# Kernel tuning notes

Hardware: AMD Instinct MI355X
Metric: run time of the kernel (lower is better)

Reference implementation:

```python
import jax, jax.numpy as jnp
import numpy as np

B, C_IN, H, W = 4, 256, 256, 256
L = 5000                 # candidate lines per image
N_PTS0, N_PTS1 = 32, 8   # sampled points per line, pooled points
DIM_LOI, DIM_FC = 128, 1024
N_OUT_LINE = 2500


def setup_inputs() -> dict:
    key = jax.random.key(0)
    ks = jax.random.split(key, 8)
    feature = jax.random.normal(ks[0], (B, C_IN, H, W), jnp.float32)
    # line endpoints in [0, 255) pixel coords (row, col)
    lines_in = jax.random.uniform(ks[1], (B, L, 2, 2), jnp.float32) * 255.0
    fc1_w = jax.random.normal(ks[2], (DIM_LOI, C_IN), jnp.float32) * 0.05
    fc1_b = jnp.zeros((DIM_LOI,), jnp.float32)
    w1 = jax.random.normal(ks[3], (DIM_FC, DIM_LOI * N_PTS1), jnp.float32) * 0.02
    b1 = jnp.zeros((DIM_FC,), jnp.float32)
    w2 = jax.random.normal(ks[4], (DIM_FC, DIM_FC), jnp.float32) * 0.02
    b2 = jnp.zeros((DIM_FC,), jnp.float32)
    w3 = jax.random.normal(ks[5], (4, DIM_FC), jnp.float32) * 0.02
    b3 = jnp.zeros((4,), jnp.float32)
    return dict(feature=feature, lines_in=lines_in, fc1_w=fc1_w, fc1_b=fc1_b,
                w1=w1, b1=b1, w2=w2, b2=b2, w3=w3, b3=b3)


def _bilinear_sample(xi, px, py):
    # xi: [C, H, W]; px, py: [P] float coords. Matches torch clamp(0, 255).
    px0 = jnp.clip(jnp.floor(px), 0.0, 255.0)
    py0 = jnp.clip(jnp.floor(py), 0.0, 255.0)
    px1 = jnp.clip(px0 + 1.0, 0.0, 255.0)
    py1 = jnp.clip(py0 + 1.0, 0.0, 255.0)
    px0l, py0l = px0.astype(jnp.int32), py0.astype(jnp.int32)
    px1l, py1l = px1.astype(jnp.int32), py1.astype(jnp.int32)
    xp = (xi[:, px0l, py0l] * (px1 - px) * (py1 - py)
          + xi[:, px1l, py0l] * (px - px0) * (py1 - py)
          + xi[:, px0l, py1l] * (px1 - px) * (py - py0)
          + xi[:, px1l, py1l] * (px - px0) * (py - py0))
    return xp  # [C, P]


def _select(p0, s0, m):
    # p0: [L,2,2], s0: [L,4], m: [L] bool. Threshold-masked, argsort by argmax
    # class (descending), cyclically padded to N_OUT_LINE.
    max_idx = jnp.argmax(s0, axis=1)
    sort_key = jnp.where(m, max_idx, -1)          # unmasked rows sink to the end
    order = jnp.argsort(-sort_key)                # stable, descending by class id
    cnt = m.sum()
    idxs = jnp.arange(N_OUT_LINE) % jnp.maximum(cnt, 1)
    sel = order[idxs]
    li = jnp.where(cnt > 0, p0[sel], jnp.zeros_like(p0[sel]))
    si = jnp.where(cnt > 0, s0[sel], jnp.zeros_like(s0[sel]))
    return li, si


def reference(feature, lines_in, fc1_w, fc1_b, w1, b1, w2, b2, w3, b3):
    # fc1: 1x1 conv -> [B, DIM_LOI, H, W]
    x = jnp.einsum('bchw,oc->bohw', feature, fc1_w) + fc1_b[None, :, None, None]

    # sample N_PTS0 points along each line: p0*lam + p1*(1-lam) - 0.5
    lam = jnp.linspace(0.0, 1.0, N_PTS0, dtype=jnp.float32)[:, None]  # [32,1]
    pts = lines_in[:, :, 0:1, :] * lam + lines_in[:, :, 1:2, :] * (1.0 - lam) - 0.5  # [B,L,32,2]
    px = pts[..., 0].reshape(B, -1)  # [B, L*32]
    py = pts[..., 1].reshape(B, -1)

    xp = jax.vmap(_bilinear_sample)(x, px, py)            # [B, C, L*32]
    xp = xp.reshape(B, DIM_LOI, L, N_PTS0).transpose(0, 2, 1, 3)  # [B, L, C, 32]

    # MaxPool1d(4, 4) over the point axis -> [B, L, C, 8]
    xp = xp.reshape(B, L, DIM_LOI, N_PTS1, N_PTS0 // N_PTS1).max(axis=-1)
    flat = xp.reshape(B, L, DIM_LOI * N_PTS1)

    # fc2 MLP: 1024 -> 1024 -> 1024 -> 4
    h = jax.nn.relu(jnp.einsum('blf,df->bld', flat, w1) + b1)
    h = jax.nn.relu(jnp.einsum('bld,ed->ble', h, w2) + b2)
    logits = jnp.einsum('ble,oe->blo', h, w3) + b3        # [B, L, 4]

    s = jax.nn.softmax(logits, axis=-1)
    mask = ((s[..., 1] > 0.25) | (s[..., 2] > 0.25) | (s[..., 3] > 0.25)) & (s[..., 0] < 0.25)

    lines_out, score_out = jax.vmap(_select)(lines_in, s, mask)
    return lines_out, score_out  # [B, 2500, 2, 2], [B, 2500, 4]
```

## Files before the change

### kernel.cpp

```cpp
#include <hip/hip_runtime.h>
#include <hip/hip_bf16.h>
#include <math.h>

#define BB 4
#define C_IN 256
#define HH 256
#define WW 256
#define LL 5000
#define N_PTS0 32
#define N_PTS1 8
#define DIM_LOI 128
#define DIM_FC 1024
#define N_OUT_LINE 2500
#define MM (BB * LL)
#define PIX (HH * WW)

typedef __attribute__((ext_vector_type(8))) short short8_t;
typedef __attribute__((ext_vector_type(4))) float float4v;

__device__ __forceinline__ short f2bf(float f) {
    union { float f; unsigned u; } c; c.f = f;
    unsigned u = c.u;
    u += 0x7FFFu + ((u >> 16) & 1u);
    return (short)(u >> 16);
}
__device__ __forceinline__ float bf2f(short h) {
    union { unsigned u; float f; } c; c.u = ((unsigned)(unsigned short)h) << 16;
    return c.f;
}

__device__ __forceinline__ void load_lds16(const void* g, void* l) {
    __builtin_amdgcn_global_load_lds(
        (const __attribute__((address_space(1))) void*)g,
        (__attribute__((address_space(3))) void*)l, 16, 0, 0);
}

__device__ __forceinline__ void wave_barrier() {
    asm volatile("" ::: "memory");
    __builtin_amdgcn_s_barrier();
    asm volatile("" ::: "memory");
}

#define MFMA_B16(a, b, c) \
    c = __builtin_amdgcn_mfma_f32_16x16x32_bf16(a, b, c, 0, 0, 0)

__global__ __launch_bounds__(256) void conv_mfma_kernel(
    const float* __restrict__ feat,
    const short* __restrict__ whi,
    const short* __restrict__ wlo,
    const float* __restrict__ bias,
    float* __restrict__ x)
{
    __shared__ short As_hi[128][40];
    __shared__ short As_lo[128][40];
    __shared__ short Ws_hi[128][40];
    __shared__ short Ws_lo[128][40];

    const int t  = threadIdx.x;
    const int m0 = blockIdx.x * 128;
    const int b  = m0 >> 16;
    const int p0 = m0 & (PIX - 1);
    const float* fb = feat + (size_t)b * C_IN * PIX + p0;

    const int w = t >> 6, lane = t & 63;
    const int wmb = (w >> 1) * 64, wnb = (w & 1) * 64;
    const int fr = lane & 15;
    const int koff = (lane >> 4) << 3;

    const int sp = t & 127;
    const int cg = t >> 7;

    float4v acc[4][4];
#pragma unroll
    for (int mi = 0; mi < 4; mi++)
#pragma unroll
        for (int ni = 0; ni < 4; ni++)
            acc[mi][ni] = (float4v){0.f, 0.f, 0.f, 0.f};

    for (int k0 = 0; k0 < C_IN; k0 += 32) {
#pragma unroll
        for (int i = 0; i < 2; i++) {
            int idx = t + (i << 8);
            int row = idx >> 2;
            int kc  = (idx & 3) << 3;
            *(int4*)&Ws_hi[row][kc] = *(const int4*)(whi + row * C_IN + k0 + kc);
            *(int4*)&Ws_lo[row][kc] = *(const int4*)(wlo + row * C_IN + k0 + kc);
        }
#pragma unroll
        for (int j = 0; j < 8; j++) {
            int c = cg * 16 + j * 2;
            float v0 = fb[(size_t)(k0 + c) * PIX + sp];
            float v1 = fb[(size_t)(k0 + c + 1) * PIX + sp];
            short h0 = f2bf(v0), h1 = f2bf(v1);
            short l0 = f2bf(v0 - bf2f(h0)), l1 = f2bf(v1 - bf2f(h1));
            *(unsigned*)&As_hi[sp][c] =
                (unsigned)(unsigned short)h0 | ((unsigned)(unsigned short)h1 << 16);
            *(unsigned*)&As_lo[sp][c] =
                (unsigned)(unsigned short)l0 | ((unsigned)(unsigned short)l1 << 16);
        }
        __syncthreads();

        short8_t ah[4], al[4];
#pragma unroll
        for (int mi = 0; mi < 4; mi++) {
            ah[mi] = *(const short8_t*)&As_hi[wmb + mi * 16 + fr][koff];
            al[mi] = *(const short8_t*)&As_lo[wmb + mi * 16 + fr][koff];
        }
#pragma unroll
        for (int ni = 0; ni < 4; ni++) {
            short8_t bh = *(const short8_t*)&Ws_hi[wnb + ni * 16 + fr][koff];
            short8_t bl = *(const short8_t*)&Ws_lo[wnb + ni * 16 + fr][koff];
#pragma unroll
            for (int mi = 0; mi < 4; mi++) {
                MFMA_B16(ah[mi], bh, acc[mi][ni]);
                MFMA_B16(al[mi], bh, acc[mi][ni]);
                MFMA_B16(ah[mi], bl, acc[mi][ni]);
            }
        }
        __syncthreads();
    }

#pragma unroll
    for (int ni = 0; ni < 4; ni++) {
        int ncol = wnb + ni * 16 + fr;
        float bv = bias[ncol];
#pragma unroll
        for (int mi = 0; mi < 4; mi++) {
            int r0 = m0 + wmb + mi * 16 + ((lane >> 4) << 2);
#pragma unroll
            for (int i2 = 0; i2 < 4; i2++) {
                x[(size_t)(r0 + i2) * 128 + ncol] = acc[mi][ni][i2] + bv;
            }
        }
    }
}

__global__ __launch_bounds__(256) void sample_pool_kernel(
    const float* __restrict__ lines,
    const float* __restrict__ x,
    short* __restrict__ phi,
    short* __restrict__ plo)
{
    const int t  = threadIdx.x;
    const int bl = blockIdx.x * 8 + (t >> 5);
    const int b  = bl / LL;
    const int cg = t & 31;
    const float* lp = lines + (size_t)bl * 4;
    const float p0r = lp[0], p0c = lp[1], p1r = lp[2], p1c = lp[3];
    const float* xb = x + (size_t)b * PIX * 128 + cg * 4;

    short8_t vh[4], vl[4];
#pragma unroll
    for (int g = 0; g < 8; g++) {
        float mx0 = -INFINITY, mx1 = -INFINITY, mx2 = -INFINITY, mx3 = -INFINITY;
#pragma unroll
        for (int j = 0; j < 4; j++) {
            int tt = g * 4 + j;
            float lam = (float)((double)tt / 31.0);
            float px = p0r * lam + p1r * (1.0f - lam) - 0.5f;
            float py = p0c * lam + p1c * (1.0f - lam) - 0.5f;
            float px0 = fminf(fmaxf(floorf(px), 0.0f), 255.0f);
            float py0 = fminf(fmaxf(floorf(py), 0.0f), 255.0f);
            float px1 = fminf(px0 + 1.0f, 255.0f);
            float py1 = fminf(py0 + 1.0f, 255.0f);
            int ix0 = (int)px0, iy0 = (int)py0, ix1 = (int)px1, iy1 = (int)py1;
            float wx1 = px1 - px, wx0 = px - px0;
            float wy1 = py1 - py, wy0 = py - py0;
            float w00 = wx1 * wy1, w10 = wx0 * wy1;
            float w01 = wx1 * wy0, w11 = wx0 * wy0;
            float4 v00 = *(const float4*)(xb + (size_t)(ix0 * WW + iy0) * 128);
            float4 v10 = *(const float4*)(xb + (size_t)(ix1 * WW + iy0) * 128);
            float4 v01 = *(const float4*)(xb + (size_t)(ix0 * WW + iy1) * 128);
            float4 v11 = *(const float4*)(xb + (size_t)(ix1 * WW + iy1) * 128);
            mx0 = fmaxf(mx0, v00.x * w00 + v10.x * w10 + v01.x * w01 + v11.x * w11);
            mx1 = fmaxf(mx1, v00.y * w00 + v10.y * w10 + v01.y * w01 + v11.y * w11);
            mx2 = fmaxf(mx2, v00.z * w00 + v10.z * w10 + v01.z * w01 + v11.z * w11);
            mx3 = fmaxf(mx3, v00.w * w00 + v10.w * w10 + v01.w * w01 + v11.w * w11);
        }
        float mxs[4] = {mx0, mx1, mx2, mx3};
#pragma unroll
        for (int k = 0; k < 4; k++) {
            short h = f2bf(mxs[k]);
            vh[k][g] = h;
            vl[k][g] = f2bf(mxs[k] - bf2f(h));
        }
    }
#pragma unroll
    for (int k = 0; k < 4; k++) {
        *(short8_t*)(phi + (size_t)bl * 1024 + (cg * 4 + k) * 8) = vh[k];
        *(short8_t*)(plo + (size_t)bl * 1024 + (cg * 4 + k) * 8) = vl[k];
    }
}

__global__ __launch_bounds__(256) void split_kernel(
    const float* __restrict__ w, short* __restrict__ hi, short* __restrict__ lo)
{
    const int i = (blockIdx.x * 256 + threadIdx.x) * 4;
    float4 v = *(const float4*)(w + i);
    float vv[4] = {v.x, v.y, v.z, v.w};
    short4 h, l;
    short hs[4], ls[4];
#pragma unroll
    for (int j = 0; j < 4; j++) {
        hs[j] = f2bf(vv[j]);
        ls[j] = f2bf(vv[j] - bf2f(hs[j]));
    }
    h.x = hs[0]; h.y = hs[1]; h.z = hs[2]; h.w = hs[3];
    l.x = ls[0]; l.y = ls[1]; l.z = ls[2]; l.w = ls[3];
    *(short4*)(hi + i) = h;
    *(short4*)(lo + i) = l;
}

#define NT 32
#define BUFS 28672
#define A_LO 6144
#define B_HI 12288
#define B_LO 20480

template <bool SPLIT_OUT>
__global__ __launch_bounds__(512, 2) void gemm_bf16x3_v4(
    const short* __restrict__ Ahi, const short* __restrict__ Alo,
    const short* __restrict__ Bhi, const short* __restrict__ Blo,
    const float* __restrict__ bias,
    float* __restrict__ Cf, short* __restrict__ Chi, short* __restrict__ Clo,
    int M, int Mtiles)
{
    __shared__ short lds[2 * BUFS];

    const int t   = threadIdx.x;
    const int bid = blockIdx.x;
    const int nwg = Mtiles * 4;
    const int q = nwg >> 3, r = nwg & 7;
    const int xcd = bid & 7, seq = bid >> 3;
    const int wgid = ((xcd < r) ? xcd * (q + 1) : r * (q + 1) + (xcd - r) * q) + seq;
    const int tileM = wgid >> 2, tileN = wgid & 3;
    const int m0 = tileM * 192, n0 = tileN * 256;

    const int w = t >> 6, lane = t & 63;
    const int wr = w >> 2;
    const int wc = w & 3;
    const int fr = lane & 15;
    const int ksw = (((lane >> 4) ^ ((lane >> 1) & 3)) << 3);
    const int a_row = wr * 96 + fr;
    const int b_row = wc * 64 + fr;

    const short* gp[7];
    int lp[7];
    {
        const int csrc = (lane & 3) ^ ((lane >> 3) & 3);
#pragma unroll
        for (int s = 0; s < 7; s++) {
            int e = w * 7 + s;
            const short* mp; int mo, j, grow;
            int rl = lane >> 2;
            if (e < 12)      { mp = Ahi; mo = 0;    j = e;      grow = min(m0 + j * 16 + rl, M - 1); }
            else if (e < 24) { mp = Alo; mo = A_LO; j = e - 12; grow = min(m0 + j * 16 + rl, M - 1); }
            else if (e < 40) { mp = Bhi; mo = B_HI; j = e - 24; grow = n0 + j * 16 + rl; }
            else             { mp = Blo; mo = B_LO; j = e - 40; grow = n0 + j * 16 + rl; }
            gp[s] = mp + (size_t)grow * 1024 + csrc * 8;
            lp[s] = mo + j * 512 + lane * 8;
        }
    }

#pragma unroll
    for (int s = 0; s < 7; s++) { load_lds16(gp[s], &lds[lp[s]]); gp[s] += 32; }
#pragma unroll
    for (int s = 0; s < 7; s++) { load_lds16(gp[s], &lds[BUFS + lp[s]]); gp[s] += 32; }
    asm volatile("s_waitcnt vmcnt(7)" ::: "memory");
    wave_barrier();

    float4v acc[6][4];
#pragma unroll
    for (int mf = 0; mf < 6; mf++)
#pragma unroll
        for (int nf = 0; nf < 4; nf++)
            acc[mf][nf] = (float4v){0.f, 0.f, 0.f, 0.f};

    for (int kt = 0; kt < NT; ++kt) {
        const int off = (kt & 1) * BUFS;

        short8_t bh[4], bl[4];
#pragma unroll
        for (int nf = 0; nf < 4; nf++) {
            bh[nf] = *(const short8_t*)&lds[off + B_HI + (b_row + nf * 16) * 32 + ksw];
            bl[nf] = *(const short8_t*)&lds[off + B_LO + (b_row + nf * 16) * 32 + ksw];
        }
#pragma unroll
        for (int mf = 0; mf < 6; mf++) {
            short8_t ah = *(const short8_t*)&lds[off + (a_row + mf * 16) * 32 + ksw];
            short8_t al = *(const short8_t*)&lds[off + A_LO + (a_row + mf * 16) * 32 + ksw];
#pragma unroll
            for (int nf = 0; nf < 4; nf++) {
                MFMA_B16(ah, bh[nf], acc[mf][nf]);
                MFMA_B16(al, bh[nf], acc[mf][nf]);
                MFMA_B16(ah, bl[nf], acc[mf][nf]);
            }
        }

        if (kt < NT - 1) {
            wave_barrier();
            if (kt + 2 < NT) {
#pragma unroll
                for (int s = 0; s < 7; s++) {
                    load_lds16(gp[s], &lds[off + lp[s]]); gp[s] += 32;
                }
                asm volatile("s_waitcnt vmcnt(7)" ::: "memory");
            } else {
                asm volatile("s_waitcnt vmcnt(0)" ::: "memory");
            }
            wave_barrier();
        }
    }

#pragma unroll
    for (int nf = 0; nf < 4; nf++) {
        int ncol = n0 + wc * 64 + nf * 16 + fr;
        float bv = bias[ncol];
#pragma unroll
        for (int mf = 0; mf < 6; mf++) {
            int r0 = m0 + wr * 96 + mf * 16 + ((lane >> 4) << 2);
#pragma unroll
            for (int i2 = 0; i2 < 4; i2++) {
                int rr = r0 + i2;
                if (rr < M) {
                    float v = fmaxf(acc[mf][nf][i2] + bv, 0.0f);
                    if (SPLIT_OUT) {
                        short h = f2bf(v);
                        Chi[(size_t)rr * 1024 + ncol] = h;
                        Clo[(size_t)rr * 1024 + ncol] = f2bf(v - bf2f(h));
                    } else {
                        Cf[(size_t)rr * 1024 + ncol] = v;
                    }
                }
            }
        }
    }
}

__global__ __launch_bounds__(256) void fc3_softmax_kernel(
    const float* __restrict__ h2, const float* __restrict__ w3,
    const float* __restrict__ b3, float* __restrict__ s, int* __restrict__ keys)
{
    const int m = blockIdx.x * 4 + (threadIdx.x >> 6);
    const int lane = threadIdx.x & 63;
    const float* hp = h2 + (size_t)m * DIM_FC;
    float a0 = 0.f, a1 = 0.f, a2 = 0.f, a3 = 0.f;
    for (int k = lane; k < DIM_FC; k += 64) {
        float hv = hp[k];
        a0 = fmaf(hv, w3[k], a0);
        a1 = fmaf(hv, w3[DIM_FC + k], a1);
        a2 = fmaf(hv, w3[2 * DIM_FC + k], a2);
        a3 = fmaf(hv, w3[3 * DIM_FC + k], a3);
    }
#pragma unroll
    for (int off = 32; off > 0; off >>= 1) {
        a0 += __shfl_down(a0, off, 64);
        a1 += __shfl_down(a1, off, 64);
        a2 += __shfl_down(a2, off, 64);
        a3 += __shfl_down(a3, off, 64);
    }
    if (lane == 0) {
        float l0 = a0 + b3[0], l1 = a1 + b3[1], l2 = a2 + b3[2], l3 = a3 + b3[3];
        float mxl = fmaxf(fmaxf(l0, l1), fmaxf(l2, l3));
        float e0 = expf(l0 - mxl), e1 = expf(l1 - mxl);
        float e2 = expf(l2 - mxl), e3 = expf(l3 - mxl);
        float inv = 1.0f / (e0 + e1 + e2 + e3);
        float s0 = e0 * inv, s1 = e1 * inv, s2 = e2 * inv, s3 = e3 * inv;
        float* sp = s + (size_t)m * 4;
        sp[0] = s0; sp[1] = s1; sp[2] = s2; sp[3] = s3;
        int best = 0; float bv = s0;
        if (s1 > bv) { best = 1; bv = s1; }
        if (s2 > bv) { best = 2; bv = s2; }
        if (s3 > bv) { best = 3; bv = s3; }
        bool msk = ((s1 > 0.25f) || (s2 > 0.25f) || (s3 > 0.25f)) && (s0 < 0.25f);
        keys[m] = msk ? best : -1;
    }
}

__global__ __launch_bounds__(64) void order_kernel(
    const int* __restrict__ keys, int* __restrict__ ord, int* __restrict__ cnts)
{
    const int b = blockIdx.x;
    const int lane = threadIdx.x;
    const int* kb = keys + b * LL;
    int c0 = 0, c1 = 0, c2 = 0, c3 = 0;
    for (int line = lane; line < LL; line += 64) {
        int k = kb[line];
        c0 += (k == 0); c1 += (k == 1); c2 += (k == 2); c3 += (k == 3);
    }
#pragma unroll
    for (int off = 32; off > 0; off >>= 1) {
        c0 += __shfl_down(c0, off, 64);
        c1 += __shfl_down(c1, off, 64);
        c2 += __shfl_down(c2, off, 64);
        c3 += __shfl_down(c3, off, 64);
    }
    int t0 = __shfl(c0, 0, 64), t1 = __shfl(c1, 0, 64);
    int t2 = __shfl(c2, 0, 64), t3 = __shfl(c3, 0, 64);
    if (lane == 0) cnts[b] = t0 + t1 + t2 + t3;
    int base[4];
    base[3] = 0; base[2] = t3; base[1] = t3 + t2; base[0] = t3 + t2 + t1;
    int run[4] = {0, 0, 0, 0};
    const unsigned long long below = (1ull << lane) - 1ull;
    int* ob = ord + b * LL;
    for (int s0 = 0; s0 < LL; s0 += 64) {
        int line = s0 + lane;
        int k = (line < LL) ? kb[line] : -2;
#pragma unroll
        for (int kk = 0; kk < 4; kk++) {
            unsigned long long mask = __ballot(k == kk);
            if (k == kk) {
                int pos = base[kk] + run[kk] + __popcll(mask & below);
                ob[pos] = line;
            }
            run[kk] += __popcll(mask);
        }
    }
}

__global__ __launch_bounds__(256) void fill_kernel(
    const float* __restrict__ lines, const float* __restrict__ s,
    const int* __restrict__ ord, const int* __restrict__ cnts,
    float* __restrict__ out)
{
    const int i = blockIdx.x * 256 + threadIdx.x;
    if (i >= BB * N_OUT_LINE) return;
    const int b = i / N_OUT_LINE;
    const int j = i % N_OUT_LINE;
    const int cnt = cnts[b];
    float4 lo = {0.f, 0.f, 0.f, 0.f}, sc = {0.f, 0.f, 0.f, 0.f};
    if (cnt > 0) {
        int line = ord[b * LL + (j % cnt)];
        lo = *(const float4*)(lines + ((size_t)b * LL + line) * 4);
        sc = *(const float4*)(s + ((size_t)b * LL + line) * 4);
    }
    *(float4*)(out + (size_t)i * 4) = lo;
    *(float4*)(out + (size_t)(BB * N_OUT_LINE) * 4 + (size_t)i * 4) = sc;
}

extern "C" void kernel_launch(void* const* d_in, const int* in_sizes, int n_in,
                              void* d_out, int out_size, void* d_ws, size_t ws_size,
                              hipStream_t stream) {
    (void)in_sizes; (void)n_in; (void)out_size; (void)ws_size;
    const float* feature = (const float*)d_in[0];
    const float* lines   = (const float*)d_in[1];
    const float* fc1_w   = (const float*)d_in[2];
    const float* fc1_b   = (const float*)d_in[3];
    const float* w1      = (const float*)d_in[4];
    const float* b1      = (const float*)d_in[5];
    const float* w2      = (const float*)d_in[6];
    const float* b2      = (const float*)d_in[7];
    const float* w3      = (const float*)d_in[8];
    const float* b3      = (const float*)d_in[9];
    float* out = (float*)d_out;

    float* x = (float*)d_ws;
    short* pooled_hi = (short*)(x + (size_t)BB * PIX * 128);
    short* pooled_lo = pooled_hi + (size_t)MM * DIM_FC;
    short* h1hi = (short*)x;
    short* h1lo = h1hi + (size_t)MM * DIM_FC;
    float* h2 = (float*)pooled_hi;
    short* w1hi = (short*)((char*)d_ws + 100u * 1024u * 1024u);
    short* w1lo = w1hi + DIM_FC * DIM_FC;
    short* w2hi = w1lo + DIM_FC * DIM_FC;
    short* w2lo = w2hi + DIM_FC * DIM_FC;
    float* s    = (float*)(pooled_lo + (size_t)MM * DIM_FC);
    int* keys   = (int*)(s + MM * 4);
    int* ord    = keys + MM;
    int* cnts   = ord + MM;
    short* fc1hi = (short*)(cnts + 64);
    short* fc1lo = fc1hi + DIM_LOI * C_IN;

    split_kernel<<<(DIM_LOI * C_IN) / 1024, 256, 0, stream>>>(fc1_w, fc1hi, fc1lo);
    conv_mfma_kernel<<<(BB * PIX) / 128, 256, 0, stream>>>(
        feature, fc1hi, fc1lo, fc1_b, x);
    sample_pool_kernel<<<MM / 8, 256, 0, stream>>>(lines, x, pooled_hi, pooled_lo);
    split_kernel<<<DIM_FC * DIM_FC / 1024, 256, 0, stream>>>(w1, w1hi, w1lo);
    split_kernel<<<DIM_FC * DIM_FC / 1024, 256, 0, stream>>>(w2, w2hi, w2lo);

    const int Mtiles = (MM + 191) / 192;
    gemm_bf16x3_v4<true><<<Mtiles * 4, 512, 0, stream>>>(
        pooled_hi, pooled_lo, w1hi, w1lo, b1, nullptr, h1hi, h1lo, MM, Mtiles);
    gemm_bf16x3_v4<false><<<Mtiles * 4, 512, 0, stream>>>(
        h1hi, h1lo, w2hi, w2lo, b2, h2, nullptr, nullptr, MM, Mtiles);

    fc3_softmax_kernel<<<MM / 4, 256, 0, stream>>>(h2, w3, b3, s, keys);
    order_kernel<<<BB, 64, 0, stream>>>(keys, ord, cnts);
    fill_kernel<<<(BB * N_OUT_LINE + 255) / 256, 256, 0, stream>>>(
        lines, s, ord, cnts, out);
}
```

Measured before the change: 898.8 us.

## Bucket-sort sampling groups spatially for cache locality in bilinear gather

Splits the per-line sampling into per-pooled-group work items and orders them by a counting sort over 32x32 spatial tiles per image, so that wavefronts gathering from the feature map touch nearby pixels and hit in cache more often. The pooled feature layout becomes group-major (g*128+channel), and the w1 weight split is permuted to match so the first GEMM result is unchanged. This adds four small kernels (histogram, scan, scatter) and atomics, and turns the pooled stores into short4 writes instead of short8 writes.

New measurement: 1.081 ms. 1.2x slower.

```diff
diff --git a/kernel.cpp b/kernel.cpp
--- a/kernel.cpp
+++ b/kernel.cpp
@@ -14,6 +14,7 @@
 #define N_OUT_LINE 2500
 #define MM (BB * LL)
 #define PIX (HH * WW)
+#define NGRP (MM * N_PTS1)
 
 typedef __attribute__((ext_vector_type(8))) short short8_t;
 typedef __attribute__((ext_vector_type(4))) float float4v;
@@ -135,61 +136,111 @@
     }
 }
 
+__global__ __launch_bounds__(256) void zero_hist_kernel(int* __restrict__ hist)
+{
+    hist[threadIdx.x] = 0;
+}
+
+__global__ __launch_bounds__(256) void group_key_kernel(
+    const float* __restrict__ lines, int* __restrict__ key, int* __restrict__ hist)
+{
+    const int gid = blockIdx.x * 256 + threadIdx.x;
+    if (gid >= NGRP) return;
+    const int bl = gid >> 3, g = gid & 7;
+    const float* lp = lines + (size_t)bl * 4;
+    const float lam = (float)((double)(g * 4) / 31.0);
+    float px = lp[0] * lam + lp[2] * (1.0f - lam) - 0.5f;
+    float py = lp[1] * lam + lp[3] * (1.0f - lam) - 0.5f;
+    int ix = min(max((int)floorf(px), 0), 255);
+    int iy = min(max((int)floorf(py), 0), 255);
+    const int b = bl / LL;
+    const int k = b * 64 + (ix >> 5) * 8 + (iy >> 5);
+    key[gid] = k;
+    atomicAdd(&hist[k], 1);
+}
+
+__global__ __launch_bounds__(256) void scan_kernel(
+    const int* __restrict__ hist, int* __restrict__ cursor)
+{
+    __shared__ int sh[256];
+    const int t = threadIdx.x;
+    const int h = hist[t];
+    sh[t] = h;
+    __syncthreads();
+#pragma unroll
+    for (int off = 1; off < 256; off <<= 1) {
+        int u = (t >= off) ? sh[t - off] : 0;
+        __syncthreads();
+        sh[t] += u;
+        __syncthreads();
+    }
+    cursor[t] = sh[t] - h;
+}
+
+__global__ __launch_bounds__(256) void scatter_kernel(
+    const int* __restrict__ key, int* __restrict__ cursor, int* __restrict__ perm)
+{
+    const int gid = blockIdx.x * 256 + threadIdx.x;
+    if (gid >= NGRP) return;
+    const int k = key[gid];
+    const int pos = atomicAdd(&cursor[k], 1);
+    perm[pos] = gid;
+}
+
 __global__ __launch_bounds__(256) void sample_pool_kernel(
     const float* __restrict__ lines,
     const float* __restrict__ x,
+    const int* __restrict__ perm,
     short* __restrict__ phi,
     short* __restrict__ plo)
 {
     const int t  = threadIdx.x;
-    const int bl = blockIdx.x * 8 + (t >> 5);
+    const int pg = perm[blockIdx.x * 8 + (t >> 5)];
+    const int bl = pg >> 3, g = pg & 7;
     const int b  = bl / LL;
     const int cg = t & 31;
     const float* lp = lines + (size_t)bl * 4;
     const float p0r = lp[0], p0c = lp[1], p1r = lp[2], p1c = lp[3];
     const float* xb = x + (size_t)b * PIX * 128 + cg * 4;
 
-    short8_t vh[4], vl[4];
-#pragma unroll
-    for (int g = 0; g < 8; g++) {
-        float mx0 = -INFINITY, mx1 = -INFINITY, mx2 = -INFINITY, mx3 = -INFINITY;
-#pragma unroll
-        for (int j = 0; j < 4; j++) {
-            int tt = g * 4 + j;
-            float lam = (float)((double)tt / 31.0);
-            float px = p0r * lam + p1r * (1.0f - lam) - 0.5f;
-            float py = p0c * lam + p1c * (1.0f - lam) - 0.5f;
-            float px0 = fminf(fmaxf(floorf(px), 0.0f), 255.0f);
-            float py0 = fminf(fmaxf(floorf(py), 0.0f), 255.0f);
-            float px1 = fminf(px0 + 1.0f, 255.0f);
-            float py1 = fminf(py0 + 1.0f, 255.0f);
-            int ix0 = (int)px0, iy0 = (int)py0, ix1 = (int)px1, iy1 = (int)py1;
-            float wx1 = px1 - px, wx0 = px - px0;
-            float wy1 = py1 - py, wy0 = py - py0;
-            float w00 = wx1 * wy1, w10 = wx0 * wy1;
-            float w01 = wx1 * wy0, w11 = wx0 * wy0;
-            float4 v00 = *(const float4*)(xb + (size_t)(ix0 * WW + iy0) * 128);
-            float4 v10 = *(const float4*)(xb + (size_t)(ix1 * WW + iy0) * 128);
-            float4 v01 = *(const float4*)(xb + (size_t)(ix0 * WW + iy1) * 128);
-            float4 v11 = *(const float4*)(xb + (size_t)(ix1 * WW + iy1) * 128);
-            mx0 = fmaxf(mx0, v00.x * w00 + v10.x * w10 + v01.x * w01 + v11.x * w11);
-            mx1 = fmaxf(mx1, v00.y * w00 + v10.y * w10 + v01.y * w01 + v11.y * w11);
-            mx2 = fmaxf(mx2, v00.z * w00 + v10.z * w10 + v01.z * w01 + v11.z * w11);
-            mx3 = fmaxf(mx3, v00.w * w00 + v10.w * w10 + v01.w * w01 + v11.w * w11);
-        }
-        float mxs[4] = {mx0, mx1, mx2, mx3};
-#pragma unroll
-        for (int k = 0; k < 4; k++) {
-            short h = f2bf(mxs[k]);
-            vh[k][g] = h;
-            vl[k][g] = f2bf(mxs[k] - bf2f(h));
-        }
-    }
+    float mx0 = -INFINITY, mx1 = -INFINITY, mx2 = -INFINITY, mx3 = -INFINITY;
+#pragma unroll
+    for (int j = 0; j < 4; j++) {
+        int tt = g * 4 + j;
+        float lam = (float)((double)tt / 31.0);
+        float px = p0r * lam + p1r * (1.0f - lam) - 0.5f;
+        float py = p0c * lam + p1c * (1.0f - lam) - 0.5f;
+        float px0 = fminf(fmaxf(floorf(px), 0.0f), 255.0f);
+        float py0 = fminf(fmaxf(floorf(py), 0.0f), 255.0f);
+        float px1 = fminf(px0 + 1.0f, 255.0f);
+        float py1 = fminf(py0 + 1.0f, 255.0f);
+        int ix0 = (int)px0, iy0 = (int)py0, ix1 = (int)px1, iy1 = (int)py1;
+        float wx1 = px1 - px, wx0 = px - px0;
+        float wy1 = py1 - py, wy0 = py - py0;
+        float w00 = wx1 * wy1, w10 = wx0 * wy1;
+        float w01 = wx1 * wy0, w11 = wx0 * wy0;
+        float4 v00 = *(const float4*)(xb + (size_t)(ix0 * WW + iy0) * 128);
+        float4 v10 = *(const float4*)(xb + (size_t)(ix1 * WW + iy0) * 128);
+        float4 v01 = *(const float4*)(xb + (size_t)(ix0 * WW + iy1) * 128);
+        float4 v11 = *(const float4*)(xb + (size_t)(ix1 * WW + iy1) * 128);
+        mx0 = fmaxf(mx0, v00.x * w00 + v10.x * w10 + v01.x * w01 + v11.x * w11);
+        mx1 = fmaxf(mx1, v00.y * w00 + v10.y * w10 + v01.y * w01 + v11.y * w11);
+        mx2 = fmaxf(mx2, v00.z * w00 + v10.z * w10 + v01.z * w01 + v11.z * w11);
+        mx3 = fmaxf(mx3, v00.w * w00 + v10.w * w10 + v01.w * w01 + v11.w * w11);
+    }
+    float mxs[4] = {mx0, mx1, mx2, mx3};
+    short4 h4, l4;
+    short hs[4], ls[4];
 #pragma unroll
     for (int k = 0; k < 4; k++) {
-        *(short8_t*)(phi + (size_t)bl * 1024 + (cg * 4 + k) * 8) = vh[k];
-        *(short8_t*)(plo + (size_t)bl * 1024 + (cg * 4 + k) * 8) = vl[k];
-    }
+        hs[k] = f2bf(mxs[k]);
+        ls[k] = f2bf(mxs[k] - bf2f(hs[k]));
+    }
+    h4.x = hs[0]; h4.y = hs[1]; h4.z = hs[2]; h4.w = hs[3];
+    l4.x = ls[0]; l4.y = ls[1]; l4.z = ls[2]; l4.w = ls[3];
+    const size_t o = (size_t)bl * 1024 + g * 128 + cg * 4;
+    *(short4*)(phi + o) = h4;
+    *(short4*)(plo + o) = l4;
 }
 
 __global__ __launch_bounds__(256) void split_kernel(
@@ -198,6 +249,29 @@
     const int i = (blockIdx.x * 256 + threadIdx.x) * 4;
     float4 v = *(const float4*)(w + i);
     float vv[4] = {v.x, v.y, v.z, v.w};
+    short4 h, l;
+    short hs[4], ls[4];
+#pragma unroll
+    for (int j = 0; j < 4; j++) {
+        hs[j] = f2bf(vv[j]);
+        ls[j] = f2bf(vv[j] - bf2f(hs[j]));
+    }
+    h.x = hs[0]; h.y = hs[1]; h.z = hs[2]; h.w = hs[3];
+    l.x = ls[0]; l.y = ls[1]; l.z = ls[2]; l.w = ls[3];
+    *(short4*)(hi + i) = h;
+    *(short4*)(lo + i) = l;
+}
+
+__global__ __launch_bounds__(256) void split_permute_kernel(
+    const float* __restrict__ w, short* __restrict__ hi, short* __restrict__ lo)
+{
+    const int i = (blockIdx.x * 256 + threadIdx.x) * 4;
+    const int d = i >> 10, kp = i & 1023;
+    const int g = kp >> 7, ch = kp & 127;
+    float vv[4];
+#pragma unroll
+    for (int j = 0; j < 4; j++)
+        vv[j] = w[(size_t)d * 1024 + (ch + j) * 8 + g];
     short4 h, l;
     short hs[4], ls[4];
 #pragma unroll
@@ -470,12 +544,21 @@
     int* cnts   = ord + MM;
     short* fc1hi = (short*)(cnts + 64);
     short* fc1lo = fc1hi + DIM_LOI * C_IN;
+    int* skey  = (int*)(fc1lo + DIM_LOI * C_IN);
+    int* sperm = skey + NGRP;
+    int* shist = sperm + NGRP;
+    int* scur  = shist + 256;
 
     split_kernel<<<(DIM_LOI * C_IN) / 1024, 256, 0, stream>>>(fc1_w, fc1hi, fc1lo);
+    zero_hist_kernel<<<1, 256, 0, stream>>>(shist);
+    group_key_kernel<<<(NGRP + 255) / 256, 256, 0, stream>>>(lines, skey, shist);
+    scan_kernel<<<1, 256, 0, stream>>>(shist, scur);
+    scatter_kernel<<<(NGRP + 255) / 256, 256, 0, stream>>>(skey, scur, sperm);
     conv_mfma_kernel<<<(BB * PIX) / 128, 256, 0, stream>>>(
         feature, fc1hi, fc1lo, fc1_b, x);
-    sample_pool_kernel<<<MM / 8, 256, 0, stream>>>(lines, x, pooled_hi, pooled_lo);
-    split_kernel<<<DIM_FC * DIM_FC / 1024, 256, 0, stream>>>(w1, w1hi, w1lo);
+    sample_pool_kernel<<<NGRP / 8, 256, 0, stream>>>(
+        lines, x, sperm, pooled_hi, pooled_lo);
+    split_permute_kernel<<<DIM_FC * DIM_FC / 1024, 256, 0, stream>>>(w1, w1hi, w1lo);
     split_kernel<<<DIM_FC * DIM_FC / 1024, 256, 0, stream>>>(w2, w2hi, w2lo);
 
     const int Mtiles = (MM + 191) / 192;
```
